# Kernel tuning notes

Hardware: AMD Instinct MI355X
Metric: run time of the kernel (lower is better)

The kernel has to match this reference:

```python
import jax, jax.numpy as jnp
import numpy as np

B, T, C, H = 4, 2048, 1024, 16
D = C // H  # head dim = 64


def setup_inputs() -> dict:
    key = jax.random.key(0)
    k0, k1, k2, k3, k4 = jax.random.split(key, 5)
    s = 0.02
    return {
        "x": jax.random.normal(k0, (B, T, C), dtype=jnp.float32),
        "W_qkv": jax.random.normal(k1, (C, 3 * C), dtype=jnp.float32) * s,
        "b_qkv": jnp.zeros((3 * C,), dtype=jnp.float32),
        "W_out": jax.random.normal(k2, (C, C), dtype=jnp.float32) * s,
        "b_out": jnp.zeros((C,), dtype=jnp.float32),
    }


def reference(x, W_qkv, b_qkv, W_out, b_out):
    b, t, c = x.shape
    qkv = x @ W_qkv + b_qkv                              # [B,T,3C]
    q, k, v = jnp.split(qkv, 3, axis=-1)
    # [B,T,C] -> [B,H,T,D]
    q = q.reshape(b, t, H, D).transpose(0, 2, 1, 3)
    k = k.reshape(b, t, H, D).transpose(0, 2, 1, 3)
    v = v.reshape(b, t, H, D).transpose(0, 2, 1, 3)
    scale = 1.0 / jnp.sqrt(jnp.asarray(D, dtype=q.dtype))
    attn = jnp.einsum("bhqd,bhkd->bhqk", q, k) * scale   # [B,H,T,T]
    causal = jnp.tril(jnp.ones((t, t), dtype=bool))
    attn = jnp.where(causal[None, None], attn, -jnp.inf)
    attn = jax.nn.softmax(attn, axis=-1)
    y = jnp.einsum("bhqk,bhkd->bhqd", attn, v)           # [B,H,T,D]
    y = y.transpose(0, 2, 1, 3).reshape(b, t, c)          # [B,T,C]
    return y @ W_out + b_out
```

## Files before the change

kernel.cpp:

```cpp
#include <hip/hip_runtime.h>
#include <math.h>

typedef __bf16 bf16x8 __attribute__((ext_vector_type(8)));
typedef __bf16 bf16x4 __attribute__((ext_vector_type(4)));
typedef short shortx4 __attribute__((ext_vector_type(4)));
typedef float floatx4 __attribute__((ext_vector_type(4)));

#define Tc 2048
#define Cdim 1024
#define Hc 16
#define Dc 64
#define Mrows 8192

__device__ __forceinline__ float bf2f(ushort u) {
  union { float f; unsigned int i; } v; v.i = ((unsigned int)u) << 16; return v.f;
}
__device__ __forceinline__ ushort f2bf(float f) {
  union { float f; unsigned int i; } v; v.f = f;
  unsigned int r = (v.i + 0x7FFFu + ((v.i >> 16) & 1u)) >> 16;
  return (ushort)r;
}
__device__ __forceinline__ ushort f2bf_pos(float f) {
  union { float f; unsigned int i; } v; v.f = f;
  return (ushort)((v.i + 0x8000u) >> 16);
}
__device__ __forceinline__ float exp2_fast(float x) {
#if __has_builtin(__builtin_amdgcn_exp2f)
  return __builtin_amdgcn_exp2f(x);
#else
  return exp2f(x);
#endif
}

#if __has_builtin(__builtin_amdgcn_mfma_f32_16x16x16_bf16)
__device__ __forceinline__ floatx4 mfma16(bf16x4 a, bf16x4 b, floatx4 c) {
  return __builtin_amdgcn_mfma_f32_16x16x16_bf16(a, b, c, 0, 0, 0);
}
#elif __has_builtin(__builtin_amdgcn_mfma_f32_16x16x16bf16_1k)
__device__ __forceinline__ floatx4 mfma16(bf16x4 a, bf16x4 b, floatx4 c) {
  union { bf16x4 bv; shortx4 sv; } ua, ub;
  ua.bv = a; ub.bv = b;
  return __builtin_amdgcn_mfma_f32_16x16x16bf16_1k(ua.sv, ub.sv, c, 0, 0, 0);
}
#else
__device__ __forceinline__ floatx4 mfma16(bf16x4 a, bf16x4 b, floatx4 c) {
  floatx4 d;
  asm("v_mfma_f32_16x16x16_bf16 %0, %1, %2, %3" : "=v"(d) : "v"(a), "v"(b), "v"(c));
  return d;
}
#endif

#if __has_builtin(__builtin_amdgcn_global_load_lds)
#define HAVE_GLL 1
__device__ __forceinline__ void async_load16(const ushort* g, ushort* l) {
  __builtin_amdgcn_global_load_lds((const __attribute__((address_space(1))) void*)g,
                                   (__attribute__((address_space(3))) void*)l, 16, 0, 0);
}
#else
#define HAVE_GLL 0
#endif

__global__ void sniff_kernel(const unsigned int* __restrict__ x, int* __restrict__ flag) {
  __shared__ int cnt;
  if (threadIdx.x == 0) cnt = 0;
  __syncthreads();
  int local = 0;
  for (int i = threadIdx.x; i < 1024; i += 256) {
    unsigned int w = x[i];
    unsigned int e = (w >> 7) & 0xFFu;
    if (e >= 100u && e <= 140u) local++;
  }
  atomicAdd(&cnt, local);
  __syncthreads();
  if (threadIdx.x == 0) *flag = (cnt >= 614) ? 1 : 0;
}

__global__ void convert_vec(const void* __restrict__ src, ushort* __restrict__ dst,
                            size_t n, const int* __restrict__ flag) {
  size_t i = (size_t)blockIdx.x * blockDim.x + threadIdx.x;
  size_t base = i * 4;
  if (base >= n) return;
  if (*flag) {
    *(ushort4*)(dst + base) = ((const ushort4*)src)[i];
  } else {
    float4 f = ((const float4*)src)[i];
    dst[base + 0] = f2bf(f.x);
    dst[base + 1] = f2bf(f.y);
    dst[base + 2] = f2bf(f.z);
    dst[base + 3] = f2bf(f.w);
  }
}

__global__ void transpose_convert(const void* __restrict__ src, ushort* __restrict__ dst,
                                  int R, int Ccols, const int* __restrict__ flag) {
  __shared__ float tile[32][33];
  const int bx = blockIdx.x, by = blockIdx.y;
  const int tx = threadIdx.x, ty = threadIdx.y;
  const bool isbf = (*flag != 0);
  #pragma unroll
  for (int i = ty; i < 32; i += 8) {
    int r = by * 32 + i;
    int c = bx * 32 + tx;
    float v = isbf ? bf2f(((const ushort*)src)[(size_t)r * Ccols + c])
                   : ((const float*)src)[(size_t)r * Ccols + c];
    tile[i][tx] = v;
  }
  __syncthreads();
  #pragma unroll
  for (int i = ty; i < 32; i += 8) {
    int cc = bx * 32 + i;
    int rr = by * 32 + tx;
    dst[(size_t)cc * R + rr] = f2bf(tile[tx][i]);
  }
}

#if HAVE_GLL
#define STAGE16(gsrc, ldst, s) async_load16((gsrc), (ldst))
#else
#define STAGE16(gsrc, ldst, s) (*(uint4*)((ldst) + ((s) & 63) * 8) = *(const uint4*)(gsrc))
#endif

#define GEMM_CORE(A_, Bt_, acc_)                                               \
  __shared__ __align__(16) ushort As[2][128 * 64];                             \
  __shared__ __align__(16) ushort Bs[2][128 * 64];                             \
  const int tid = threadIdx.x;                                                 \
  const int wave = tid >> 6, lane = tid & 63;                                  \
  const int col = lane & 15, quad = lane >> 4;                                 \
  const int m0 = blockIdx.y * 128, n0 = blockIdx.x * 128;                      \
  const int wm = (wave >> 1) * 64, wn = (wave & 1) * 64;                       \
  floatx4 acc_[4][4];                                                          \
  _Pragma("unroll") for (int i = 0; i < 4; ++i)                                \
    _Pragma("unroll") for (int j = 0; j < 4; ++j)                              \
      acc_[i][j] = (floatx4){0.f, 0.f, 0.f, 0.f};                              \
  auto stage_ = [&](int t) {                                                   \
    const int bb = t & 1;                                                      \
    _Pragma("unroll") for (int i = 0; i < 4; ++i) {                            \
      const int sbase = i * 256 + wave * 64;                                   \
      const int s = sbase + lane;                                              \
      const int r = s >> 3, g = (lane & 7) ^ (r & 7);                          \
      STAGE16(A_ + (size_t)(m0 + r) * 1024 + t * 64 + g * 8,                   \
              As[bb] + sbase * 8, s);                                          \
      STAGE16(Bt_ + (size_t)(n0 + r) * 1024 + t * 64 + g * 8,                  \
              Bs[bb] + sbase * 8, s);                                          \
    }                                                                          \
  };                                                                           \
  stage_(0);                                                                   \
  __syncthreads();                                                             \
  for (int t = 0; t < 16; ++t) {                                               \
    if (t + 1 < 16) stage_(t + 1);                                             \
    const ushort* Ab = As[t & 1];                                              \
    const ushort* Bb = Bs[t & 1];                                              \
    _Pragma("unroll") for (int ks = 0; ks < 2; ++ks) {                         \
      bf16x8 af[4], bfv[4];                                                    \
      _Pragma("unroll") for (int mi = 0; mi < 4; ++mi) {                       \
        const int rr = wm + mi * 16 + col;                                     \
        const int gg = (ks * 4 + quad) ^ (rr & 7);                             \
        af[mi] = *(const bf16x8*)(Ab + rr * 64 + gg * 8);                      \
      }                                                                        \
      _Pragma("unroll") for (int ni = 0; ni < 4; ++ni) {                       \
        const int rr = wn + ni * 16 + col;                                     \
        const int gg = (ks * 4 + quad) ^ (rr & 7);                             \
        bfv[ni] = *(const bf16x8*)(Bb + rr * 64 + gg * 8);                     \
      }                                                                        \
      _Pragma("unroll") for (int mi = 0; mi < 4; ++mi)                         \
        _Pragma("unroll") for (int ni = 0; ni < 4; ++ni)                       \
          acc_[mi][ni] = __builtin_amdgcn_mfma_f32_16x16x32_bf16(              \
              af[mi], bfv[ni], acc_[mi][ni], 0, 0, 0);                         \
    }                                                                          \
    __syncthreads();                                                           \
  }

__global__ __launch_bounds__(256) void gemm_qkv(const ushort* __restrict__ A,
                                                const ushort* __restrict__ Bt,
                                                const ushort* __restrict__ bias,
                                                ushort* __restrict__ Qb,
                                                ushort* __restrict__ Kb,
                                                ushort* __restrict__ Vtb) {
  GEMM_CORE(A, Bt, acc)
  #pragma unroll
  for (int ni = 0; ni < 4; ++ni) {
    const int n = n0 + wn + ni * 16 + col;
    const float bi = bf2f(bias[n]);
    const int which = n >> 10;
    const int within = n & 1023;
    const int h = within >> 6, d = within & 63;
    #pragma unroll
    for (int mi = 0; mi < 4; ++mi) {
      #pragma unroll
      for (int r = 0; r < 4; ++r) {
        const int row = m0 + wm + mi * 16 + quad * 4 + r;
        const float v = acc[mi][ni][r] + bi;
        const int b = row >> 11, t = row & 2047;
        const size_t hb = (size_t)(b * Hc + h);
        const ushort ub = f2bf(v);
        if (which == 0)      Qb[(hb * Tc + t) * Dc + d] = ub;
        else if (which == 1) Kb[(hb * Tc + t) * Dc + d] = ub;
        else                 Vtb[(hb * Dc + d) * Tc + t] = ub;
      }
    }
  }
}

__global__ __launch_bounds__(256) void gemm_out(const ushort* __restrict__ A,
                                                const ushort* __restrict__ Bt,
                                                const ushort* __restrict__ bias,
                                                void* __restrict__ out,
                                                const int* __restrict__ flag) {
  GEMM_CORE(A, Bt, acc)
  const bool isbf = (*flag != 0);
  #pragma unroll
  for (int ni = 0; ni < 4; ++ni) {
    const int n = n0 + wn + ni * 16 + col;
    const float bi = bf2f(bias[n]);
    #pragma unroll
    for (int mi = 0; mi < 4; ++mi) {
      #pragma unroll
      for (int r = 0; r < 4; ++r) {
        const int row = m0 + wm + mi * 16 + quad * 4 + r;
        const float v = acc[mi][ni][r] + bi;
        const size_t idx = (size_t)row * 1024 + n;
        if (isbf) ((ushort*)out)[idx] = f2bf(v);
        else      ((float*)out)[idx] = v;
      }
    }
  }
}

__global__ __launch_bounds__(512, 4) void attn_mfma(const ushort* __restrict__ Qb,
                                                    const ushort* __restrict__ Kb,
                                                    const ushort* __restrict__ Vtb,
                                                    ushort* __restrict__ Yb) {
  __shared__ __align__(16) ushort Kl[2][4096];
  __shared__ __align__(16) ushort Vl[2][4096];
  const int tid = threadIdx.x;
  const int bh = blockIdx.y;
  const int wave = tid >> 6, lane = tid & 63;
  const int col = lane & 15, quad = lane >> 4;
  const int pair = blockIdx.x;
  const int pHI = 15 - pair;
  const int pLO = pair;
  const int nA = 2 * pHI + 2;
  const int ntot = nA + 2 * pLO + 2;

  const ushort* Qh = Qb + (size_t)bh * Tc * Dc;
  const ushort* Kh = Kb + (size_t)bh * Tc * Dc;
  const ushort* Vth = Vtb + (size_t)bh * Dc * Tc;

  const int sr = tid >> 3, sg = (tid & 7) ^ (sr & 7);
  const ushort* kg = Kh + (size_t)sr * Dc + sg * 8;
  const ushort* vg = Vth + (size_t)sr * Tc + sg * 8;

  const int q0A = pHI * 128 + wave * 16;
  const int q0B = pLO * 128 + wave * 16;
  const int cdA = 2 * pHI + (wave >> 2);
  const int cdB = 2 * pLO + (wave >> 2);
  const int ktw = wave & 3;

  bf16x8 qfA[2], qfB[2];
  {
    const ushort* qa = Qh + (size_t)(q0A + col) * Dc + quad * 8;
    qfA[0] = *(const bf16x8*)(qa);
    qfA[1] = *(const bf16x8*)(qa + 32);
    const ushort* qb = Qh + (size_t)(q0B + col) * Dc + quad * 8;
    qfB[0] = *(const bf16x8*)(qb);
    qfB[1] = *(const bf16x8*)(qb + 32);
  }

  floatx4 o[4];
  float lpart = 0.f;
  #pragma unroll
  for (int dt = 0; dt < 4; ++dt) o[dt] = (floatx4){0.f, 0.f, 0.f, 0.f};

  constexpr float C1 = 0.18033688f;
  constexpr float C2 = -17.312340f;
  const int b = bh >> 4, h = bh & 15;

  auto stage = [&](int gi) {
    const int p = gi & 1;
    const int c = (gi < nA) ? gi : gi - nA;
    const size_t kOff = (size_t)c * 64;
#if HAVE_GLL
    async_load16(kg + kOff * Dc, &Kl[p][wave * 512]);
    async_load16(vg + kOff, &Vl[p][wave * 512]);
#else
    *(uint4*)&Kl[p][tid * 8] = *(const uint4*)(kg + kOff * Dc);
    *(uint4*)&Vl[p][tid * 8] = *(const uint4*)(vg + kOff);
#endif
  };

  auto chunk_compute = [&](int c, int p, const bf16x8 (&qf)[2], int cd) {
    if (c > cd) return;
    const bool masked = (c == cd);
    #pragma unroll
    for (int kt = 0; kt < 4; ++kt) {
      if (masked && kt > ktw) continue;
      const int rowk = kt * 16 + col;
      const int swk = rowk & 7;
      bf16x8 ka0 = *(const bf16x8*)(&Kl[p][rowk * 64 + ((quad ^ swk) * 8)]);
      bf16x8 ka1 = *(const bf16x8*)(&Kl[p][rowk * 64 + (((quad + 4) ^ swk) * 8)]);
      bf16x4 vf[4];
      #pragma unroll
      for (int dt = 0; dt < 4; ++dt) {
        const int rowv = dt * 16 + col;
        const int gv = (2 * kt + (quad >> 1)) ^ (rowv & 7);
        vf[dt] = *(const bf16x4*)(&Vl[p][rowv * 64 + gv * 8 + (quad & 1) * 4]);
      }
      floatx4 sf = {0.f, 0.f, 0.f, 0.f};
      sf = __builtin_amdgcn_mfma_f32_16x16x32_bf16(ka0, qf[0], sf, 0, 0, 0);
      sf = __builtin_amdgcn_mfma_f32_16x16x32_bf16(ka1, qf[1], sf, 0, 0, 0);
      union { ushort u[4]; bf16x4 v; } pu;
      float ps = 0.f;
      const bool tri = masked && (kt == ktw);
      #pragma unroll
      for (int r = 0; r < 4; ++r) {
        float pe = exp2_fast(fmaf(sf[r], C1, C2));
        if (tri) pe = (quad * 4 + r <= col) ? pe : 0.f;
        ps += pe;
        pu.u[r] = f2bf_pos(pe);
      }
      lpart += ps;
      #pragma unroll
      for (int dt = 0; dt < 4; ++dt)
        o[dt] = mfma16(vf[dt], pu.v, o[dt]);
    }
  };

  auto flush = [&](int q0) {
    float l = lpart;
    l += __shfl_xor(l, 16);
    l += __shfl_xor(l, 32);
    const float inv = 1.f / l;
    const int q = q0 + col;
    const size_t base = ((size_t)b * Tc + q) * Cdim + h * Dc;
    #pragma unroll
    for (int dt = 0; dt < 4; ++dt) {
      ushort4 y;
      y.x = f2bf(o[dt][0] * inv);
      y.y = f2bf(o[dt][1] * inv);
      y.z = f2bf(o[dt][2] * inv);
      y.w = f2bf(o[dt][3] * inv);
      *(ushort4*)(Yb + base + dt * 16 + quad * 4) = y;
    }
  };

  stage(0);
  __syncthreads();

  for (int c = 0; c < nA; ++c) {
    if (c + 1 < ntot) stage(c + 1);
    chunk_compute(c, c & 1, qfA, cdA);
    if (c == nA - 1) {
      flush(q0A);
      lpart = 0.f;
      #pragma unroll
      for (int dt = 0; dt < 4; ++dt) o[dt] = (floatx4){0.f, 0.f, 0.f, 0.f};
    }
    __syncthreads();
  }
  for (int gi = nA; gi < ntot; ++gi) {
    if (gi + 1 < ntot) stage(gi + 1);
    chunk_compute(gi - nA, gi & 1, qfB, cdB);
    __syncthreads();
  }
  flush(q0B);
}

extern "C" void kernel_launch(void* const* d_in, const int* in_sizes, int n_in,
                              void* d_out, int out_size, void* d_ws, size_t ws_size,
                              hipStream_t stream) {
  const void* x    = d_in[0];
  const void* Wqkv = d_in[1];
  const void* bqkv = d_in[2];
  const void* Wout = d_in[3];
  const void* bout = d_in[4];

  char* ws = (char*)d_ws;
  size_t off = 0;
  auto alloc = [&](size_t bytes) { size_t r = off; off += (bytes + 255) & ~(size_t)255; return r; };

  int*    flag = (int*)   (ws + alloc(256));
  ushort* xb   = (ushort*)(ws + alloc((size_t)Mrows * Cdim * 2));
  ushort* wqt  = (ushort*)(ws + alloc((size_t)3 * Cdim * Cdim * 2));
  ushort* wot  = (ushort*)(ws + alloc((size_t)Cdim * Cdim * 2));
  ushort* bqb  = (ushort*)(ws + alloc((size_t)3 * Cdim * 2));
  ushort* bob  = (ushort*)(ws + alloc((size_t)Cdim * 2));
  ushort* Qb   = (ushort*)(ws + alloc((size_t)Mrows * Cdim * 2));
  ushort* Kb   = (ushort*)(ws + alloc((size_t)Mrows * Cdim * 2));
  ushort* Vtb  = (ushort*)(ws + alloc((size_t)Mrows * Cdim * 2));
  ushort* Yb   = xb;

  sniff_kernel<<<1, 256, 0, stream>>>((const unsigned int*)x, flag);

  convert_vec<<<(Mrows * Cdim) / 1024, 256, 0, stream>>>(x, xb, (size_t)Mrows * Cdim, flag);
  convert_vec<<<3, 256, 0, stream>>>(bqkv, bqb, 3 * Cdim, flag);
  convert_vec<<<1, 256, 0, stream>>>(bout, bob, Cdim, flag);
  transpose_convert<<<dim3(96, 32), dim3(32, 8), 0, stream>>>(Wqkv, wqt, Cdim, 3 * Cdim, flag);
  transpose_convert<<<dim3(32, 32), dim3(32, 8), 0, stream>>>(Wout, wot, Cdim, Cdim, flag);

  gemm_qkv<<<dim3(24, 64), 256, 0, stream>>>(xb, wqt, bqb, Qb, Kb, Vtb);
  attn_mfma<<<dim3(8, 64), 512, 0, stream>>>(Qb, Kb, Vtb, Yb);
  gemm_out<<<dim3(8, 64), 256, 0, stream>>>(Yb, wot, bob, d_out, flag);
}
```

Baseline: 294.5 us.

## Rework GEMM core with explicit async-load pipeline, XCD tile swizzle, and priority hints

Adds a dedicated GEMM main loop for the async global-to-LDS path. It prefetches two K tiles ahead, waits on vmcnt counters explicitly, loads all LDS fragments before a barrier, and raises wave priority around the MFMA block. Workgroup IDs are remapped in groups of 8, which is meant to improve L2 locality across chiplets. Launch bounds now request 2 blocks per CU. The point is to overlap global loads with MFMA work and cut stalls, at the cost of more hand-tuned waitcnt logic and more register pressure.

```diff
diff --git a/kernel.cpp b/kernel.cpp
--- a/kernel.cpp
+++ b/kernel.cpp
@@ -115,11 +115,78 @@
 }
 
 #if HAVE_GLL
-#define STAGE16(gsrc, ldst, s) async_load16((gsrc), (ldst))
+
+#define GEMM_CORE(A_, Bt_, acc_)                                               \
+  __shared__ __align__(16) ushort As[2][128 * 64];                             \
+  __shared__ __align__(16) ushort Bs[2][128 * 64];                             \
+  const int tid = threadIdx.x;                                                 \
+  const int wave = tid >> 6, lane = tid & 63;                                  \
+  const int col = lane & 15, quad = lane >> 4;                                 \
+  const int nwg = gridDim.x * gridDim.y;                                       \
+  const int wg = blockIdx.y * gridDim.x + blockIdx.x;                          \
+  const int swz = ((nwg & 7) == 0) ? ((wg & 7) * (nwg >> 3) + (wg >> 3)) : wg; \
+  const int bx_ = swz / gridDim.y, by_ = swz % gridDim.y;                      \
+  const int m0 = by_ * 128, n0 = bx_ * 128;                                    \
+  const int wm = (wave >> 1) * 64, wn = (wave & 1) * 64;                       \
+  floatx4 acc_[4][4];                                                          \
+  _Pragma("unroll") for (int i = 0; i < 4; ++i)                                \
+    _Pragma("unroll") for (int j = 0; j < 4; ++j)                              \
+      acc_[i][j] = (floatx4){0.f, 0.f, 0.f, 0.f};                              \
+  auto stage_ = [&](int u) {                                                   \
+    const int bb = u & 1;                                                      \
+    _Pragma("unroll") for (int i = 0; i < 4; ++i) {                            \
+      const int sbase = i * 256 + wave * 64;                                   \
+      const int s = sbase + lane;                                              \
+      const int r = s >> 3, g = (lane & 7) ^ (r & 7);                          \
+      async_load16(A_ + (size_t)(m0 + r) * 1024 + u * 64 + g * 8,              \
+                   As[bb] + sbase * 8);                                        \
+      async_load16(Bt_ + (size_t)(n0 + r) * 1024 + u * 64 + g * 8,             \
+                   Bs[bb] + sbase * 8);                                        \
+    }                                                                          \
+  };                                                                           \
+  stage_(0);                                                                   \
+  stage_(1);                                                                   \
+  asm volatile("s_waitcnt vmcnt(8)" ::: "memory");                             \
+  __builtin_amdgcn_sched_barrier(0);                                           \
+  __builtin_amdgcn_s_barrier();                                                \
+  for (int t = 0; t < 16; ++t) {                                               \
+    const ushort* Ab = As[t & 1];                                              \
+    const ushort* Bb = Bs[t & 1];                                              \
+    bf16x8 af[2][4], bfv[2][4];                                                \
+    _Pragma("unroll") for (int ks = 0; ks < 2; ++ks) {                         \
+      _Pragma("unroll") for (int mi = 0; mi < 4; ++mi) {                       \
+        const int rr = wm + mi * 16 + col;                                     \
+        const int gg = (ks * 4 + quad) ^ (rr & 7);                             \
+        af[ks][mi] = *(const bf16x8*)(Ab + rr * 64 + gg * 8);                  \
+      }                                                                        \
+      _Pragma("unroll") for (int ni = 0; ni < 4; ++ni) {                       \
+        const int rr = wn + ni * 16 + col;                                     \
+        const int gg = (ks * 4 + quad) ^ (rr & 7);                             \
+        bfv[ks][ni] = *(const bf16x8*)(Bb + rr * 64 + gg * 8);                 \
+      }                                                                        \
+    }                                                                          \
+    asm volatile("s_waitcnt lgkmcnt(0)" ::: "memory");                         \
+    __builtin_amdgcn_sched_barrier(0);                                         \
+    __builtin_amdgcn_s_barrier();                                              \
+    if (t + 2 < 16) stage_(t + 2);                                             \
+    __builtin_amdgcn_s_setprio(1);                                             \
+    _Pragma("unroll") for (int mi = 0; mi < 4; ++mi)                           \
+      _Pragma("unroll") for (int ni = 0; ni < 4; ++ni) {                       \
+        acc_[mi][ni] = __builtin_amdgcn_mfma_f32_16x16x32_bf16(                \
+            af[0][mi], bfv[0][ni], acc_[mi][ni], 0, 0, 0);                     \
+        acc_[mi][ni] = __builtin_amdgcn_mfma_f32_16x16x32_bf16(                \
+            af[1][mi], bfv[1][ni], acc_[mi][ni], 0, 0, 0);                     \
+      }                                                                        \
+    __builtin_amdgcn_s_setprio(0);                                             \
+    if (t + 2 < 16) { asm volatile("s_waitcnt vmcnt(8)" ::: "memory"); }       \
+    else            { asm volatile("s_waitcnt vmcnt(0)" ::: "memory"); }       \
+    __builtin_amdgcn_sched_barrier(0);                                         \
+    __builtin_amdgcn_s_barrier();                                              \
+  }
+
 #else
+
 #define STAGE16(gsrc, ldst, s) (*(uint4*)((ldst) + ((s) & 63) * 8) = *(const uint4*)(gsrc))
-#endif
-
 #define GEMM_CORE(A_, Bt_, acc_)                                               \
   __shared__ __align__(16) ushort As[2][128 * 64];                             \
   __shared__ __align__(16) ushort Bs[2][128 * 64];                             \
@@ -170,12 +237,14 @@
     __syncthreads();                                                           \
   }
 
-__global__ __launch_bounds__(256) void gemm_qkv(const ushort* __restrict__ A,
-                                                const ushort* __restrict__ Bt,
-                                                const ushort* __restrict__ bias,
-                                                ushort* __restrict__ Qb,
-                                                ushort* __restrict__ Kb,
-                                                ushort* __restrict__ Vtb) {
+#endif
+
+__global__ __launch_bounds__(256, 2) void gemm_qkv(const ushort* __restrict__ A,
+                                                   const ushort* __restrict__ Bt,
+                                                   const ushort* __restrict__ bias,
+                                                   ushort* __restrict__ Qb,
+                                                   ushort* __restrict__ Kb,
+                                                   ushort* __restrict__ Vtb) {
   GEMM_CORE(A, Bt, acc)
   #pragma unroll
   for (int ni = 0; ni < 4; ++ni) {
@@ -201,11 +270,11 @@
   }
 }
 
-__global__ __launch_bounds__(256) void gemm_out(const ushort* __restrict__ A,
-                                                const ushort* __restrict__ Bt,
-                                                const ushort* __restrict__ bias,
-                                                void* __restrict__ out,
-                                                const int* __restrict__ flag) {
+__global__ __launch_bounds__(256, 2) void gemm_out(const ushort* __restrict__ A,
+                                                   const ushort* __restrict__ Bt,
+                                                   const ushort* __restrict__ bias,
+                                                   void* __restrict__ out,
+                                                   const int* __restrict__ flag) {
   GEMM_CORE(A, Bt, acc)
   const bool isbf = (*flag != 0);
   #pragma unroll
```

Measured after the change: 304.1 us. +3.2%, slower.
